# Performance work log

Hardware: AMD Instinct MI355X
Metric: run time of the kernel (lower is better)

## Reference

```python
import jax, jax.numpy as jnp
import numpy as np

B, N, C, H = 8, 1025, 512, 8
G = 32  # grid size; S = G*G = N-1


def setup_inputs() -> dict:
    key = jax.random.key(0)
    ks = jax.random.split(key, 5)
    return {
        "x": jax.random.normal(ks[0], (B, N, C), dtype=jnp.float32),
        "qkv_w": jax.random.normal(ks[1], (3 * C, C), dtype=jnp.float32) * (C ** -0.5),
        "proj_w": jax.random.normal(ks[2], (C, C), dtype=jnp.float32) * (C ** -0.5),
        "proj_b": jnp.zeros((C,), dtype=jnp.float32),
        "wg_w": jax.random.normal(ks[3], (H, 64), dtype=jnp.float32) * 0.125,
        "wg_b": jnp.zeros((H,), dtype=jnp.float32),
    }


def _geometry_bias(wg_w, wg_b):
    # BoxRelationalEmbedding on a fixed 32x32 grid; batch-independent, so computed once.
    S = G * G
    xs = jnp.arange(G, dtype=jnp.float32)
    px = jnp.repeat(xs, G)   # px_min: row index per flattened cell
    py = jnp.tile(xs, G)     # py_min: col index per flattened cell
    rx0, ry0 = px / G, py / G
    rx1, ry1 = (px + 1.0) / G, (py + 1.0) / G
    cx = 0.5 * (rx0 + rx1)
    cy = 0.5 * (ry0 + ry1)
    w = rx1 - rx0 + 1.0
    h = ry1 - ry0 + 1.0
    dx = jnp.log(jnp.clip(jnp.abs((cx[:, None] - cx[None, :]) / w[:, None]), 1e-3, None))
    dy = jnp.log(jnp.clip(jnp.abs((cy[:, None] - cy[None, :]) / h[:, None]), 1e-3, None))
    dw = jnp.log(w[:, None] / w[None, :])
    dh = jnp.log(h[:, None] / h[None, :])
    pos = jnp.stack([dx, dy, dw, dh], axis=-1)  # [S,S,4]
    dim_mat = 1.0 / jnp.power(1000.0, jnp.arange(8, dtype=jnp.float32) / 8.0)  # dim_g/8 = 8 freqs
    mul = (100.0 * pos)[..., None] * dim_mat        # [S,S,4,8]
    mul = mul.reshape(S, S, 32)
    emb = jnp.concatenate([jnp.sin(mul), jnp.cos(mul)], axis=-1)  # [S,S,64]
    rgw = jax.nn.relu(jnp.einsum('ijd,hd->hij', emb, wg_w) + wg_b[:, None, None])  # [H,S,S]
    rgw = jnp.log(jnp.clip(rgw, 1e-6, None))
    # pad zero column (dim 3 cat of t1) then zero row (dim 2 cat of t2) -> [H, S+1, S+1]
    return jnp.pad(rgw, ((0, 0), (1, 0), (1, 0)))


def reference(x, qkv_w, proj_w, proj_b, wg_w, wg_b):
    b, n, c = x.shape
    hd = c // H
    scale = hd ** -0.5
    bias = _geometry_bias(wg_w, wg_b)  # [H, n, n]
    qkv = (x @ qkv_w.T).reshape(b, n, 3, H, hd)
    q, k, v = qkv[:, :, 0], qkv[:, :, 1], qkv[:, :, 2]  # each [b,n,H,hd]
    attn = jnp.einsum('bihd,bjhd->bhij', q, k) * scale + bias[None]
    attn = jax.nn.softmax(attn, axis=-1)
    out = jnp.einsum('bhij,bjhd->bihd', attn, v).reshape(b, n, c)
    return out @ proj_w.T + proj_b
```

## Files before the change

### kernel.cpp

```cpp
#include <hip/hip_runtime.h>
#include <hip/hip_bf16.h>
#include <hip/hip_fp16.h>
#include <math.h>

#define B_  8
#define N_  1025
#define C_  512
#define H_  8
#define HD_ 64
#define M_  (B_ * N_)
#define VCS 2560
#define VST 36

typedef __attribute__((ext_vector_type(8))) short short8;
typedef __attribute__((ext_vector_type(4))) float f32x4;
typedef __attribute__((ext_vector_type(4))) unsigned short us4;

__device__ inline unsigned short bf16u(float x) {
    __hip_bfloat16 t = __float2bfloat16(x);
    return *(unsigned short*)&t;
}
__device__ inline float fexp2(float x) {
    float r;
    asm("v_exp_f32 %0, %1" : "=v"(r) : "v"(x));
    return r;
}
__device__ inline float h2f(unsigned short u) {
    __half_raw hr; hr.x = u;
    return __half2float(__half(hr));
}
__device__ inline void load_lds16(const void* g, void* l) {
    __builtin_amdgcn_global_load_lds(
        (const __attribute__((address_space(1))) unsigned int*)g,
        (__attribute__((address_space(3))) unsigned int*)l, 16, 0, 0);
}

#define PER_ ((size_t)B_ * H_ * N_ * HD_)
#define SZ_QKVW (3 * C_ * C_)
#define SZ_PRJW (C_ * C_)
#define CAST_BLKS ((4198400 + 786432 + 262144) / 4 / 256)
#define EXP_BLKS 256

__global__ void prep_kernel(const float* __restrict__ x,
                            const float* __restrict__ qkv_w,
                            const float* __restrict__ proj_w,
                            const float* __restrict__ wg_w,
                            const float* __restrict__ wg_b,
                            unsigned short* __restrict__ xb,
                            unsigned short* __restrict__ wqkvb,
                            unsigned short* __restrict__ wprjb,
                            unsigned short* __restrict__ big) {
    __shared__ float tl[1024];
    int blk = blockIdx.x;
    int tid = threadIdx.x;
    if (blk < EXP_BLKS) {
        int h = blk >> 5, rs = blk & 31;
        const float* w = wg_w + h * 64;
        float wb = wg_b[h];
#pragma unroll 1
        for (int e = tid; e < 1024; e += 256) {
            int a = e >> 5, b = e & 31;
            float dx = logf(fmaxf((float)a * (1.0f / 33.0f), 0.001f));
            float dy = logf(fmaxf((float)b * (1.0f / 33.0f), 0.001f));
            float acc = wb;
#pragma unroll
            for (int k = 0; k < 8; k++) {
                float f = powf(1000.0f, -(float)k * 0.125f);
                float X = 100.0f * dx * f;
                float Y = 100.0f * dy * f;
                acc += w[k]      * sinf(X);
                acc += w[8 + k]  * sinf(Y);
                acc += w[32 + k] * cosf(X);
                acc += w[40 + k] * cosf(Y);
                acc += w[48 + k] + w[56 + k];
            }
            tl[e] = log2f(fmaxf(fmaxf(acc, 0.0f), 1e-6f));
        }
        __syncthreads();
        int rbase = rs * 36;
#pragma unroll 1
        for (int e8 = tid; e8 < 36 * 132; e8 += 256) {
            int rr = e8 / 132;
            int cg = e8 - rr * 132;
            int r = rbase + rr;
            int c0 = cg * 8;
            int i = min(r, 1024) - 1;
            int ix = i >> 5, iy = i & 31;
            unsigned short o8[8];
#pragma unroll
            for (int e = 0; e < 8; e++) {
                int c = c0 + e;
                float v;
                if (r == 0 || c == 0) v = 0.f;
                else if (c > 1024)    v = -60000.f;
                else {
                    int j = c - 1;
                    int da = __sad(ix, j >> 5, 0u);
                    int db = __sad(iy, j & 31, 0u);
                    v = tl[da * 32 + db];
                }
                __half hv = __float2half(v);
                o8[e] = *(unsigned short*)&hv;
            }
            *(short8*)(big + ((size_t)h * 1152 + r) * 1056 + c0) = *(short8*)o8;
        }
        return;
    }
    long i4 = ((long)(blk - EXP_BLKS) * 256 + tid) * 4;
    const float* src;
    unsigned short* dst;
    long off;
    if (i4 < (long)PER_)                    { src = x;      dst = xb;    off = i4; }
    else if (i4 < (long)PER_ + SZ_QKVW)     { src = qkv_w;  dst = wqkvb; off = i4 - PER_; }
    else                                    { src = proj_w; dst = wprjb; off = i4 - PER_ - SZ_QKVW; }
    float4 v = *(const float4*)(src + off);
    ushort4 p;
    p.x = bf16u(v.x); p.y = bf16u(v.y); p.z = bf16u(v.z); p.w = bf16u(v.w);
    *(ushort4*)(dst + off) = p;
}

#define GK 512

__global__ __launch_bounds__(256) void gemm_qkv_mfma(
        const unsigned short* __restrict__ A, const unsigned short* __restrict__ W,
        unsigned short* __restrict__ qb, unsigned short* __restrict__ kb,
        unsigned short* __restrict__ vtc) {
    __shared__ __align__(16) unsigned short As[128 * 32];
    __shared__ __align__(16) unsigned short Bs[128 * 32];
    int tid = threadIdx.x;
    int w = tid >> 6, lane = tid & 63;
    int quad = lane >> 4, l16 = lane & 15;
    int m0 = blockIdx.y * 128;
    int n0 = blockIdx.x * 128;
    int wr = (w >> 1) * 64, wc = (w & 1) * 64;

    int c0 = tid, c1 = tid + 256;
    int a_r0 = min(m0 + (c0 >> 2), M_ - 1), a_c0 = (c0 & 3) * 8;
    int a_r1 = min(m0 + (c1 >> 2), M_ - 1), a_c1 = (c1 & 3) * 8;
    int b_r0 = n0 + (c0 >> 2), b_r1 = n0 + (c1 >> 2);

    int which = n0 >> 9;
    int h = ((n0 + wc) >> 6) & 7;

    f32x4 acc[4][4];
    const f32x4 zero4 = {0.f, 0.f, 0.f, 0.f};
#pragma unroll
    for (int mi = 0; mi < 4; mi++)
#pragma unroll
        for (int ni = 0; ni < 4; ni++) acc[mi][ni] = zero4;

    for (int k0 = 0; k0 < GK; k0 += 32) {
        __syncthreads();
        load_lds16(A + (size_t)a_r0 * GK + k0 + a_c0, &As[w * 512]);
        load_lds16(A + (size_t)a_r1 * GK + k0 + a_c1, &As[2048 + w * 512]);
        load_lds16(W + (size_t)b_r0 * GK + k0 + a_c0, &Bs[w * 512]);
        load_lds16(W + (size_t)b_r1 * GK + k0 + a_c1, &Bs[2048 + w * 512]);
        __syncthreads();
        short8 af[4], bf[4];
#pragma unroll
        for (int mi = 0; mi < 4; mi++)
            af[mi] = *(const short8*)&As[(wr + mi * 16 + l16) * 32 + quad * 8];
#pragma unroll
        for (int ni = 0; ni < 4; ni++)
            bf[ni] = *(const short8*)&Bs[(wc + ni * 16 + l16) * 32 + quad * 8];
#pragma unroll
        for (int mi = 0; mi < 4; mi++)
#pragma unroll
            for (int ni = 0; ni < 4; ni++)
                acc[mi][ni] = __builtin_amdgcn_mfma_f32_16x16x32_bf16(
                    bf[ni], af[mi], acc[mi][ni], 0, 0, 0);
    }

    if (which < 2) {
        unsigned short* dst = (which == 0) ? qb : kb;
        float sc = (which == 0) ? 0.18033688f : 1.0f;
#pragma unroll
        for (int mi = 0; mi < 4; mi++) {
            int m = m0 + wr + mi * 16 + l16;
            if (m < M_) {
                int bb = m / N_;
                int i  = m - bb * N_;
                unsigned short* row = dst + ((size_t)(bb * H_ + h) * N_ + i) * HD_;
#pragma unroll
                for (int ni = 0; ni < 4; ni++) {
                    ushort4 pk;
                    pk.x = bf16u(acc[mi][ni][0] * sc);
                    pk.y = bf16u(acc[mi][ni][1] * sc);
                    pk.z = bf16u(acc[mi][ni][2] * sc);
                    pk.w = bf16u(acc[mi][ni][3] * sc);
                    *(ushort4*)(row + ni * 16 + quad * 4) = pk;
                }
            }
        }
    } else {
#pragma unroll
        for (int mi = 0; mi < 4; mi++) {
            int m = m0 + wr + mi * 16 + l16;
            if (m < M_) {
                int bb = m / N_;
                int i  = m - bb * N_;
                int ch = i >> 5, key = i & 31;
                int slot = ((key >> 2) & 3) * 8 + ((key >> 4) << 2) + (key & 3);
                unsigned short* base = vtc + ((size_t)(bb * H_ + h) * VST + ch) * VCS + slot;
#pragma unroll
                for (int ni = 0; ni < 4; ni++)
#pragma unroll
                    for (int reg = 0; reg < 4; reg++)
                        base[(ni * 16 + quad * 4 + reg) * 40] = bf16u(acc[mi][ni][reg]);
            }
        }
    }
}

__global__ __launch_bounds__(256) void gemm_proj_mfma(
        const unsigned short* __restrict__ A, const unsigned short* __restrict__ W,
        const float* __restrict__ bias, float* __restrict__ out) {
    __shared__ __align__(16) unsigned short As[128 * 32];
    __shared__ __align__(16) unsigned short Bs[128 * 32];
    int tid = threadIdx.x;
    int w = tid >> 6, lane = tid & 63;
    int quad = lane >> 4, l16 = lane & 15;
    int m0 = blockIdx.y * 128;
    int n0 = blockIdx.x * 128;
    int wr = (w >> 1) * 64, wc = (w & 1) * 64;

    int c0 = tid, c1 = tid + 256;
    int a_r0 = min(m0 + (c0 >> 2), M_ - 1), a_c0 = (c0 & 3) * 8;
    int a_r1 = min(m0 + (c1 >> 2), M_ - 1), a_c1 = (c1 & 3) * 8;
    int b_r0 = n0 + (c0 >> 2), b_r1 = n0 + (c1 >> 2);

    f32x4 acc[4][4];
    const f32x4 zero4 = {0.f, 0.f, 0.f, 0.f};
#pragma unroll
    for (int mi = 0; mi < 4; mi++)
#pragma unroll
        for (int ni = 0; ni < 4; ni++) acc[mi][ni] = zero4;

    for (int k0 = 0; k0 < GK; k0 += 32) {
        __syncthreads();
        load_lds16(A + (size_t)a_r0 * GK + k0 + a_c0, &As[w * 512]);
        load_lds16(A + (size_t)a_r1 * GK + k0 + a_c1, &As[2048 + w * 512]);
        load_lds16(W + (size_t)b_r0 * GK + k0 + a_c0, &Bs[w * 512]);
        load_lds16(W + (size_t)b_r1 * GK + k0 + a_c1, &Bs[2048 + w * 512]);
        __syncthreads();
        short8 af[4], bf[4];
#pragma unroll
        for (int mi = 0; mi < 4; mi++)
            af[mi] = *(const short8*)&As[(wr + mi * 16 + l16) * 32 + quad * 8];
#pragma unroll
        for (int ni = 0; ni < 4; ni++)
            bf[ni] = *(const short8*)&Bs[(wc + ni * 16 + l16) * 32 + quad * 8];
#pragma unroll
        for (int mi = 0; mi < 4; mi++)
#pragma unroll
            for (int ni = 0; ni < 4; ni++)
                acc[mi][ni] = __builtin_amdgcn_mfma_f32_16x16x32_bf16(
                    af[mi], bf[ni], acc[mi][ni], 0, 0, 0);
    }

    float bvals[4];
#pragma unroll
    for (int ni = 0; ni < 4; ni++) bvals[ni] = bias[n0 + wc + ni * 16 + l16];
#pragma unroll
    for (int mi = 0; mi < 4; mi++)
#pragma unroll
        for (int reg = 0; reg < 4; reg++) {
            int m = m0 + wr + mi * 16 + quad * 4 + reg;
            if (m < M_) {
                float* row = out + (size_t)m * C_ + n0 + wc;
#pragma unroll
                for (int ni = 0; ni < 4; ni++)
                    row[ni * 16 + l16] = acc[mi][ni][reg] + bvals[ni];
            }
        }
}

#define RT_ 144

__global__ __launch_bounds__(576, 4) void attn_fused(
        const unsigned short* __restrict__ qg,
        const unsigned short* __restrict__ kg,
        const unsigned short* __restrict__ vtc,
        const unsigned short* __restrict__ bigtab,
        unsigned short* __restrict__ ob) {
    __shared__ __align__(16) unsigned short Ks[2][6144];
    __shared__ __align__(16) unsigned short Vs[2][7680];

    int tid = threadIdx.x;
    int w = tid >> 6, lane = tid & 63;
    int quad = lane >> 4, l16 = lane & 15;

    int lin = blockIdx.x;
    int xcd = lin & 7;
    int u = lin >> 3;
    int bhi = u & 7;
    int mt = u >> 3;
    int bh = xcd * 8 + bhi;
    int b = bh >> 3, h = bh & 7;

    const unsigned short* qp = qg + (size_t)bh * N_ * HD_;
    const unsigned short* kp = kg + (size_t)bh * N_ * HD_;
    const unsigned short* vp = vtc + (size_t)bh * VST * VCS;

    int qrow = mt * RT_ + w * 16 + l16;
    const unsigned short* bt = bigtab + ((size_t)h * 1152 + qrow) * 1056 + quad * 4;

    short8 qf[2];
    {
        int row = min(qrow, N_ - 1);
        qf[0] = *(const short8*)(qp + (size_t)row * HD_ + quad * 8);
        qf[1] = *(const short8*)(qp + (size_t)row * HD_ + 32 + quad * 8);
    }

    f32x4 o_acc[4], l_acc;
    const f32x4 zero4 = {0.f, 0.f, 0.f, 0.f};
#pragma unroll
    for (int g2 = 0; g2 < 4; g2++) o_acc[g2] = zero4;
    l_acc = zero4;
    short8 ones;
    {
        short one_bf = (short)0x3F80;
#pragma unroll
        for (int j = 0; j < 8; j++) ones[j] = one_bf;
    }

    auto stage = [&](int t, int buf) {
#pragma unroll
        for (int r2 = 0; r2 < 3; r2++) {
            int cb = w * 3 + r2;
            if (cb < 12) {
                int ch = cb * 64 + lane;
                int ct = ch >> 7, rem = ch & 127;
                int oct = rem >> 4, k16 = rem & 15;
                int key = min(t * 96 + ct * 16 + k16, N_ - 1);
                load_lds16(kp + (size_t)key * HD_ + oct * 8, &Ks[buf][cb * 512]);
            } else {
                int vb = cb - 12;
                load_lds16(vp + (size_t)t * 3 * VCS + (size_t)(vb * 64 + lane) * 8,
                           &Vs[buf][vb * 512]);
            }
        }
    };

    us4 bcur[6], bnx[6];
#pragma unroll
    for (int i = 0; i < 6; i++)
        bnx[i] = *(const us4*)(bt + (i >> 1) * 32 + (i & 1) * 16);
    stage(0, 0);

#pragma unroll 1
    for (int t = 0; t < 11; t++) {
        int buf = t & 1;
        __syncthreads();

#pragma unroll
        for (int i = 0; i < 6; i++) bcur[i] = bnx[i];
        if (t < 10) {
            const unsigned short* btp = bt + (t + 1) * 96;
#pragma unroll
            for (int i = 0; i < 6; i++)
                bnx[i] = *(const us4*)(btp + (i >> 1) * 32 + (i & 1) * 16);
            stage(t + 1, buf ^ 1);
        }

        f32x4 s[6];
        __builtin_amdgcn_s_setprio(1);
#pragma unroll
        for (int ct = 0; ct < 6; ct++) {
            short8 kf0 = *(const short8*)&Ks[buf][(ct * 128 + quad * 16 + l16) * 8];
            short8 kf1 = *(const short8*)&Ks[buf][(ct * 128 + (4 + quad) * 16 + l16) * 8];
            s[ct] = __builtin_amdgcn_mfma_f32_16x16x32_bf16(kf0, qf[0], zero4, 0, 0, 0);
            s[ct] = __builtin_amdgcn_mfma_f32_16x16x32_bf16(kf1, qf[1], s[ct], 0, 0, 0);
        }
        __builtin_amdgcn_s_setprio(0);

#pragma unroll
        for (int ks = 0; ks < 3; ks++) {
            short8 pf;
#pragma unroll
            for (int e = 0; e < 8; e++) {
                int par = e >> 2, r = e & 3;
                float bia = h2f(bcur[ks * 2 + par][r]);
                float p = fexp2(s[ks * 2 + par][r] + bia);
                pf[e] = (short)bf16u(p);
            }
            const unsigned short* vcp = &Vs[buf][ks * 2560 + quad * 8];
            __builtin_amdgcn_s_setprio(1);
#pragma unroll
            for (int g2 = 0; g2 < 4; g2++) {
                short8 vf = *(const short8*)(vcp + (g2 * 16 + l16) * 40);
                o_acc[g2] = __builtin_amdgcn_mfma_f32_16x16x32_bf16(
                    pf, vf, o_acc[g2], 0, 0, 0);
            }
            l_acc = __builtin_amdgcn_mfma_f32_16x16x32_bf16(pf, ones, l_acc, 0, 0, 0);
            __builtin_amdgcn_s_setprio(0);
        }
    }

    int rbase = mt * RT_ + w * 16 + quad * 4;
#pragma unroll
    for (int reg = 0; reg < 4; reg++) {
        int r = rbase + reg;
        if (r < N_) {
            float inv = 1.0f / l_acc[reg];
            unsigned short* orow = ob + ((size_t)b * N_ + r) * C_ + h * HD_ + l16;
#pragma unroll
            for (int g2 = 0; g2 < 4; g2++)
                orow[g2 * 16] = bf16u(o_acc[g2][reg] * inv);
        }
    }
}

extern "C" void kernel_launch(void* const* d_in, const int* in_sizes, int n_in,
                              void* d_out, int out_size, void* d_ws, size_t ws_size,
                              hipStream_t stream) {
    const float* x      = (const float*)d_in[0];
    const float* qkv_w  = (const float*)d_in[1];
    const float* proj_w = (const float*)d_in[2];
    const float* proj_b = (const float*)d_in[3];
    const float* wg_w   = (const float*)d_in[4];
    const float* wg_b   = (const float*)d_in[5];
    float* out = (float*)d_out;

    const size_t per = PER_;
    char* ws = (char*)d_ws;
    unsigned short* bigtab = (unsigned short*)ws;
    unsigned short* xb     = bigtab + (size_t)8 * 1152 * 1056;
    unsigned short* wqkvb  = xb + per;
    unsigned short* wprjb  = wqkvb + (size_t)SZ_QKVW;
    unsigned short* qb     = wprjb + (size_t)SZ_PRJW;
    unsigned short* kb     = qb + per;
    unsigned short* vtc    = kb + per;
    unsigned short* ob     = vtc + (size_t)64 * VST * VCS;

    prep_kernel<<<EXP_BLKS + CAST_BLKS, 256, 0, stream>>>(x, qkv_w, proj_w, wg_w, wg_b,
                                                          xb, wqkvb, wprjb, bigtab);
    gemm_qkv_mfma<<<dim3(12, 65), 256, 0, stream>>>(xb, wqkvb, qb, kb, vtc);
    attn_fused<<<8 * 8 * 8, 576, 0, stream>>>(qb, kb, vtc, bigtab, ob);
    gemm_proj_mfma<<<dim3(4, 65), 256, 0, stream>>>(ob, wprjb, proj_b, out);
}
```

Baseline: 192.2 us.

## Process two query row groups per wave to reuse K/V LDS fragments

Each wave now handles 32 query rows (two 16-row groups) instead of 16, so the query tile per block doubles to 288 and the grid shrinks from 512 to 256 blocks. K and V fragments read from LDS are reused across both row groups, which halves the LDS and global K/V staging traffic per query row. The QK^T MFMAs are now interleaved per key-slice with the softmax/PV work, and the block-to-head mapping drops the XCD-aware swizzle. The costs are higher register pressure (launch bounds cut to 3 blocks per CU), fewer blocks to fill the GPU, and bias loads for the second group that are issued without prefetch.

Measured after the change: 185.2 us. 3.6% less time.

```diff
diff --git a/kernel.cpp b/kernel.cpp
--- a/kernel.cpp
+++ b/kernel.cpp
@@ -275,9 +275,9 @@
         }
 }
 
-#define RT_ 144
-
-__global__ __launch_bounds__(576, 4) void attn_fused(
+#define RT_ 288
+
+__global__ __launch_bounds__(576, 3) void attn_fused(
         const unsigned short* __restrict__ qg,
         const unsigned short* __restrict__ kg,
         const unsigned short* __restrict__ vtc,
@@ -291,32 +291,33 @@
     int quad = lane >> 4, l16 = lane & 15;
 
     int lin = blockIdx.x;
-    int xcd = lin & 7;
-    int u = lin >> 3;
-    int bhi = u & 7;
-    int mt = u >> 3;
-    int bh = xcd * 8 + bhi;
+    int bh = lin & 63;
+    int mt = lin >> 6;
     int b = bh >> 3, h = bh & 7;
 
     const unsigned short* qp = qg + (size_t)bh * N_ * HD_;
     const unsigned short* kp = kg + (size_t)bh * N_ * HD_;
     const unsigned short* vp = vtc + (size_t)bh * VST * VCS;
 
-    int qrow = mt * RT_ + w * 16 + l16;
-    const unsigned short* bt = bigtab + ((size_t)h * 1152 + qrow) * 1056 + quad * 4;
-
-    short8 qf[2];
+    int qrA = mt * RT_ + w * 32 + l16;
+    const unsigned short* btA = bigtab + ((size_t)h * 1152 + qrA) * 1056 + quad * 4;
+    const unsigned short* btB = btA + (size_t)16 * 1056;
+
+    short8 qfA[2], qfB[2];
     {
-        int row = min(qrow, N_ - 1);
-        qf[0] = *(const short8*)(qp + (size_t)row * HD_ + quad * 8);
-        qf[1] = *(const short8*)(qp + (size_t)row * HD_ + 32 + quad * 8);
-    }
-
-    f32x4 o_acc[4], l_acc;
+        int rowA = min(qrA, N_ - 1);
+        int rowB = min(qrA + 16, N_ - 1);
+        qfA[0] = *(const short8*)(qp + (size_t)rowA * HD_ + quad * 8);
+        qfA[1] = *(const short8*)(qp + (size_t)rowA * HD_ + 32 + quad * 8);
+        qfB[0] = *(const short8*)(qp + (size_t)rowB * HD_ + quad * 8);
+        qfB[1] = *(const short8*)(qp + (size_t)rowB * HD_ + 32 + quad * 8);
+    }
+
+    f32x4 oA[4], oB[4], lA, lB;
     const f32x4 zero4 = {0.f, 0.f, 0.f, 0.f};
 #pragma unroll
-    for (int g2 = 0; g2 < 4; g2++) o_acc[g2] = zero4;
-    l_acc = zero4;
+    for (int g2 = 0; g2 < 4; g2++) { oA[g2] = zero4; oB[g2] = zero4; }
+    lA = zero4; lB = zero4;
     short8 ones;
     {
         short one_bf = (short)0x3F80;
@@ -342,10 +343,10 @@
         }
     };
 
-    us4 bcur[6], bnx[6];
+    us4 bAc[6], bAn[6];
 #pragma unroll
     for (int i = 0; i < 6; i++)
-        bnx[i] = *(const us4*)(bt + (i >> 1) * 32 + (i & 1) * 16);
+        bAn[i] = *(const us4*)(btA + (i >> 1) * 32 + (i & 1) * 16);
     stage(0, 0);
 
 #pragma unroll 1
@@ -354,59 +355,86 @@
         __syncthreads();
 
 #pragma unroll
-        for (int i = 0; i < 6; i++) bcur[i] = bnx[i];
+        for (int i = 0; i < 6; i++) bAc[i] = bAn[i];
+        us4 bB[6];
+        {
+            const unsigned short* btp = btB + t * 96;
+#pragma unroll
+            for (int i = 0; i < 6; i++)
+                bB[i] = *(const us4*)(btp + (i >> 1) * 32 + (i & 1) * 16);
+        }
         if (t < 10) {
-            const unsigned short* btp = bt + (t + 1) * 96;
+            const unsigned short* btp = btA + (t + 1) * 96;
 #pragma unroll
             for (int i = 0; i < 6; i++)
-                bnx[i] = *(const us4*)(btp + (i >> 1) * 32 + (i & 1) * 16);
+                bAn[i] = *(const us4*)(btp + (i >> 1) * 32 + (i & 1) * 16);
             stage(t + 1, buf ^ 1);
         }
 
-        f32x4 s[6];
-        __builtin_amdgcn_s_setprio(1);
-#pragma unroll
-        for (int ct = 0; ct < 6; ct++) {
-            short8 kf0 = *(const short8*)&Ks[buf][(ct * 128 + quad * 16 + l16) * 8];
-            short8 kf1 = *(const short8*)&Ks[buf][(ct * 128 + (4 + quad) * 16 + l16) * 8];
-            s[ct] = __builtin_amdgcn_mfma_f32_16x16x32_bf16(kf0, qf[0], zero4, 0, 0, 0);
-            s[ct] = __builtin_amdgcn_mfma_f32_16x16x32_bf16(kf1, qf[1], s[ct], 0, 0, 0);
-        }
-        __builtin_amdgcn_s_setprio(0);
-
 #pragma unroll
         for (int ks = 0; ks < 3; ks++) {
-            short8 pf;
+            f32x4 sA[2], sB[2];
+#pragma unroll
+            for (int ctl = 0; ctl < 2; ctl++) {
+                int ct = ks * 2 + ctl;
+                short8 kf0 = *(const short8*)&Ks[buf][(ct * 128 + quad * 16 + l16) * 8];
+                short8 kf1 = *(const short8*)&Ks[buf][(ct * 128 + (4 + quad) * 16 + l16) * 8];
+                sA[ctl] = __builtin_amdgcn_mfma_f32_16x16x32_bf16(kf0, qfA[0], zero4, 0, 0, 0);
+                sA[ctl] = __builtin_amdgcn_mfma_f32_16x16x32_bf16(kf1, qfA[1], sA[ctl], 0, 0, 0);
+                sB[ctl] = __builtin_amdgcn_mfma_f32_16x16x32_bf16(kf0, qfB[0], zero4, 0, 0, 0);
+                sB[ctl] = __builtin_amdgcn_mfma_f32_16x16x32_bf16(kf1, qfB[1], sB[ctl], 0, 0, 0);
+            }
+            const unsigned short* vcp = &Vs[buf][ks * 2560 + quad * 8];
+            short8 vf[4];
+#pragma unroll
+            for (int g2 = 0; g2 < 4; g2++)
+                vf[g2] = *(const short8*)(vcp + (g2 * 16 + l16) * 40);
+
+            short8 pfA;
 #pragma unroll
             for (int e = 0; e < 8; e++) {
                 int par = e >> 2, r = e & 3;
-                float bia = h2f(bcur[ks * 2 + par][r]);
-                float p = fexp2(s[ks * 2 + par][r] + bia);
-                pf[e] = (short)bf16u(p);
-            }
-            const unsigned short* vcp = &Vs[buf][ks * 2560 + quad * 8];
+                float bia = h2f(bAc[ks * 2 + par][r]);
+                pfA[e] = (short)bf16u(fexp2(sA[par][r] + bia));
+            }
             __builtin_amdgcn_s_setprio(1);
 #pragma unroll
-            for (int g2 = 0; g2 < 4; g2++) {
-                short8 vf = *(const short8*)(vcp + (g2 * 16 + l16) * 40);
-                o_acc[g2] = __builtin_amdgcn_mfma_f32_16x16x32_bf16(
-                    pf, vf, o_acc[g2], 0, 0, 0);
-            }
-            l_acc = __builtin_amdgcn_mfma_f32_16x16x32_bf16(pf, ones, l_acc, 0, 0, 0);
+            for (int g2 = 0; g2 < 4; g2++)
+                oA[g2] = __builtin_amdgcn_mfma_f32_16x16x32_bf16(pfA, vf[g2], oA[g2], 0, 0, 0);
+            lA = __builtin_amdgcn_mfma_f32_16x16x32_bf16(pfA, ones, lA, 0, 0, 0);
             __builtin_amdgcn_s_setprio(0);
-        }
-    }
-
-    int rbase = mt * RT_ + w * 16 + quad * 4;
-#pragma unroll
-    for (int reg = 0; reg < 4; reg++) {
-        int r = rbase + reg;
-        if (r < N_) {
-            float inv = 1.0f / l_acc[reg];
-            unsigned short* orow = ob + ((size_t)b * N_ + r) * C_ + h * HD_ + l16;
+
+            short8 pfB;
+#pragma unroll
+            for (int e = 0; e < 8; e++) {
+                int par = e >> 2, r = e & 3;
+                float bia = h2f(bB[ks * 2 + par][r]);
+                pfB[e] = (short)bf16u(fexp2(sB[par][r] + bia));
+            }
+            __builtin_amdgcn_s_setprio(1);
 #pragma unroll
             for (int g2 = 0; g2 < 4; g2++)
-                orow[g2 * 16] = bf16u(o_acc[g2][reg] * inv);
+                oB[g2] = __builtin_amdgcn_mfma_f32_16x16x32_bf16(pfB, vf[g2], oB[g2], 0, 0, 0);
+            lB = __builtin_amdgcn_mfma_f32_16x16x32_bf16(pfB, ones, lB, 0, 0, 0);
+            __builtin_amdgcn_s_setprio(0);
+        }
+    }
+
+#pragma unroll
+    for (int grp = 0; grp < 2; grp++) {
+        int rbase = mt * RT_ + w * 32 + grp * 16 + quad * 4;
+        const f32x4* oX = grp ? oB : oA;
+        const f32x4& lX = grp ? lB : lA;
+#pragma unroll
+        for (int reg = 0; reg < 4; reg++) {
+            int r = rbase + reg;
+            if (r < N_) {
+                float inv = 1.0f / lX[reg];
+                unsigned short* orow = ob + ((size_t)b * N_ + r) * C_ + h * HD_ + l16;
+#pragma unroll
+                for (int g2 = 0; g2 < 4; g2++)
+                    orow[g2 * 16] = bf16u(oX[g2][reg] * inv);
+            }
         }
     }
 }
@@ -436,6 +464,6 @@
     prep_kernel<<<EXP_BLKS + CAST_BLKS, 256, 0, stream>>>(x, qkv_w, proj_w, wg_w, wg_b,
                                                           xb, wqkvb, wprjb, bigtab);
     gemm_qkv_mfma<<<dim3(12, 65), 256, 0, stream>>>(xb, wqkvb, qb, kb, vtc);
-    attn_fused<<<8 * 8 * 8, 576, 0, stream>>>(qb, kb, vtc, bigtab, ob);
+    attn_fused<<<256, 576, 0, stream>>>(qb, kb, vtc, bigtab, ob);
     gemm_proj_mfma<<<dim3(4, 65), 256, 0, stream>>>(ob, wprjb, proj_b, out);
 }
```
